# Optimization experiments

Measured on AMD Instinct MI355X. Metric: run time of the kernel, lower is better.

## Reference

```python
import jax, jax.numpy as jnp
import numpy as np

B, S, H, NH, MAXLEN = 4, 1024, 2048, 16, 1024
HD = H // NH  # head_dim = 128

def setup_inputs() -> dict:
    key = jax.random.key(0)
    ks = jax.random.split(key, 16)
    def lin(i):
        # torch Linear default init ~ U(-1/sqrt(in), 1/sqrt(in)); store W as [in, out]
        bound = 1.0 / np.sqrt(H)
        W = jax.random.uniform(ks[i], (H, H), jnp.float32, -bound, bound)
        b = jax.random.uniform(ks[i + 1], (H,), jnp.float32, -bound, bound)
        return W, b
    Wq, bq = lin(0)
    Wk, bk = lin(2)
    Wv, bv = lin(4)
    Wu, bu = lin(6)
    Wf2, bf2 = lin(8)
    rel_table = jax.random.normal(ks[10], (2 * MAXLEN - 1, NH), jnp.float32)
    query = jax.random.normal(ks[11], (B, S, H), jnp.float32)
    key_t = jax.random.normal(ks[12], (B, S, H), jnp.float32)
    value = jax.random.normal(ks[13], (B, S, H), jnp.float32)
    # causal mask [B, Sq, Sk]
    attn_mask = jnp.broadcast_to(jnp.tril(jnp.ones((S, S), bool)), (B, S, S))
    return {"query": query, "key": key_t, "value": value, "attn_mask": attn_mask,
            "Wq": Wq, "bq": bq, "Wk": Wk, "bk": bk, "Wv": Wv, "bv": bv,
            "Wu": Wu, "bu": bu, "Wf2": Wf2, "bf2": bf2, "rel_table": rel_table}

def reference(query, key, value, attn_mask, Wq, bq, Wk, bk, Wv, bv, Wu, bu, Wf2, bf2, rel_table):
    silu = jax.nn.silu
    U = silu(query @ Wu + bu)                      # [B,S,H]
    Q = silu(query @ Wq + bq).reshape(B, S, NH, HD).transpose(0, 2, 1, 3)  # [B,NH,S,HD]
    K = silu(key @ Wk + bk).reshape(B, S, NH, HD).transpose(0, 2, 1, 3)
    V = silu(value @ Wv + bv).reshape(B, S, NH, HD).transpose(0, 2, 1, 3)
    scale = HD ** -0.5
    scores = jnp.einsum('bhqd,bhkd->bhqk', Q, K) * scale  # [B,NH,S,S]
    # relative position bias lookup (non-infer path)
    positions = jnp.arange(S)[:, None] - jnp.arange(S)[None, :]
    rel_idx = positions + MAXLEN - 1                       # [S,S]
    rel_bias = rel_table[rel_idx].transpose(2, 0, 1)[None]  # [1,NH,S,S]
    scores = scores + rel_bias
    attn = silu(scores)  # SiLU attention instead of softmax
    attn = jnp.where(attn_mask[:, None, :, :], attn, 0.0)
    out = jnp.einsum('bhqk,bhkd->bhqd', attn, V)           # [B,NH,S,HD]
    out = out.transpose(0, 2, 1, 3).reshape(B, S, H)
    gated = out * U
    return gated @ Wf2 + bf2
```

## Files before the change

### kernel.cpp

```cpp
#include <hip/hip_runtime.h>
#include <stdint.h>

#define HDIM 2048
#define SEQLEN 1024
#define NHEADS 16
#define HEADD 128

typedef unsigned short u16;
typedef unsigned int u32;
typedef __attribute__((ext_vector_type(8))) short bf16x8;
typedef __attribute__((ext_vector_type(8))) u16 u16x8;
typedef __attribute__((ext_vector_type(4))) u16 u16x4;
typedef __attribute__((ext_vector_type(4))) float f32x4;

__device__ __forceinline__ float bf2f(u16 u) {
    union { u32 i; float f; } v; v.i = ((u32)u) << 16; return v.f;
}
__device__ __forceinline__ u16 f2bf(float f) {
    union { float f; u32 i; } v; v.f = f;
    return (u16)((v.i + 0x7fffu + ((v.i >> 16) & 1u)) >> 16);
}
__device__ __forceinline__ u16 f2bf_t(float f) {
    union { float f; u32 i; } v; v.f = f; return (u16)(v.i >> 16);
}
__device__ __forceinline__ float silu_f(float x) {
    return x * __builtin_amdgcn_rcpf(1.f + __expf(-x));
}
__device__ __forceinline__ void glds16(const void* g, void* l) {
    __builtin_amdgcn_global_load_lds(
        (const __attribute__((address_space(1))) u32*)g,
        (__attribute__((address_space(3))) u32*)l, 16, 0, 0);
}

__global__ __launch_bounds__(256) void f32_to_bf16(const float* __restrict__ in,
                                                   u16* __restrict__ out, int n8) {
    int i = blockIdx.x * 256 + threadIdx.x;
    const int stride = gridDim.x * 256;
    for (; i < n8; i += stride) {
        f32x4 a = *(const f32x4*)&in[(size_t)i * 8];
        f32x4 b = *(const f32x4*)&in[(size_t)i * 8 + 4];
        u16x8 o;
#pragma unroll
        for (int j = 0; j < 4; ++j) { o[j] = f2bf(a[j]); o[4 + j] = f2bf(b[j]); }
        *(u16x8*)&out[(size_t)i * 8] = o;
    }
}

__global__ __launch_bounds__(256) void transpose_w(const float* __restrict__ W,
                                                   u16* __restrict__ WT) {
    __shared__ u16 T[64][76];
    const int r0 = blockIdx.y * 64;
    const int c0 = blockIdx.x * 64;
    const int t = threadIdx.x;
#pragma unroll
    for (int c = t; c < 1024; c += 256) {
        const int r = c >> 4, cc = (c & 15) << 2;
        f32x4 v = *(const f32x4*)&W[(size_t)(r0 + r) * HDIM + c0 + cc];
        u16x4 o;
#pragma unroll
        for (int j = 0; j < 4; ++j) o[j] = f2bf(v[j]);
        *(u16x4*)&T[r][cc] = o;
    }
    __syncthreads();
#pragma unroll
    for (int c = t; c < 512; c += 256) {
        const int n = c >> 3, kc = (c & 7) << 3;
        u16x8 v;
#pragma unroll
        for (int j = 0; j < 8; ++j) v[j] = T[kc + j][n];
        *(u16x8*)&WT[(size_t)(c0 + n) * HDIM + r0 + kc] = v;
    }
}

__global__ __launch_bounds__(256) void transpose_v(const u16* __restrict__ V,
                                                   u16* __restrict__ VT) {
    __shared__ u16 T[64][76];
    const int bh = blockIdx.y;
    const int st = (blockIdx.x & 15) * 64;
    const int dt = (blockIdx.x >> 4) * 64;
    const int b = bh >> 4, h = bh & 15;
    const int t = threadIdx.x;
#pragma unroll
    for (int c = t; c < 1024; c += 256) {
        const int s = c >> 4, d4 = (c & 15) << 2;
        *(u16x4*)&T[s][d4] =
            *(const u16x4*)&V[(size_t)(b * SEQLEN + st + s) * HDIM + h * HEADD + dt + d4];
    }
    __syncthreads();
#pragma unroll
    for (int c = t; c < 512; c += 256) {
        const int d = c >> 3, s8 = (c & 7) << 3;
        u16x8 v;
#pragma unroll
        for (int j = 0; j < 8; ++j) v[j] = T[s8 + j][d];
        *(u16x8*)&VT[((size_t)bh * HEADD + dt + d) * SEQLEN + st + s8] = v;
    }
}

__global__ __launch_bounds__(512, 2) void gemm256_8p(
    const u16* __restrict__ X,
    const u16* __restrict__ WTq, const u16* __restrict__ WTu,
    const float* __restrict__ bq, const float* __restrict__ bu,
    u16* __restrict__ Qo, u16* __restrict__ Uo)
{
    extern __shared__ u16 lds[];
    const int t = threadIdx.x;
    const int lane = t & 63, wid = t >> 6;
    const int l15 = lane & 15, l4 = lane >> 4;
    const int wr = wid >> 2, wn = wid & 3;

    const int bid = blockIdx.x;
    const int u = (bid & 7) * 32 + (bid >> 3);
    const int tm = u & 15, tn = u >> 4;
    const int m0 = tm * 256;
    const int n0 = tn * 256;
    const u16* WT = (n0 < 2048) ? WTq : WTu;
    const float* bias = (n0 < 2048) ? bq : bu;
    u16* outp = (n0 < 2048) ? Qo : Uo;
    const int nc0 = n0 & 2047;

    const int r64 = t >> 3;
    const int cse = (((t & 7) ^ (r64 & 7)) << 3);
    const u16* gA = X + (size_t)(m0 + r64) * HDIM + cse;
    const int rB0 = (r64 >> 5) * 64 + (r64 & 31);
    const u16* gB = WT + (size_t)(nc0 + rB0) * HDIM + cse;

    const int wbase = wid * 512;
    const int dstBw = (wid >> 2) * 4096 + (wid & 3) * 512;

    int offA[8][2], offB[4][2];
#pragma unroll
    for (int mf = 0; mf < 8; ++mf) {
        const int row = wr * 128 + mf * 16 + l15;
#pragma unroll
        for (int kk = 0; kk < 2; ++kk) {
            const int c = kk * 4 + l4;
            offA[mf][kk] = row * 64 + (((c) ^ (row & 7)) << 3);
        }
    }
#pragma unroll
    for (int nf = 0; nf < 4; ++nf) {
        const int row = wn * 64 + nf * 16 + l15;
#pragma unroll
        for (int kk = 0; kk < 2; ++kk) {
            const int c = kk * 4 + l4;
            offB[nf][kk] = 16384 + row * 64 + (((c) ^ (row & 7)) << 3);
        }
    }

#define SA(buf, rb, kt) glds16(gA + (size_t)(rb) * HDIM + (kt) * 64, \
                               lds + (buf) * 32768 + (rb) * 64 + wbase)
#define SB(buf, c, half, kt) glds16(gB + (size_t)((c) * 128 + (half) * 32) * HDIM + (kt) * 64, \
                               lds + (buf) * 32768 + 16384 + dstBw + (c) * 8192 + (half) * 2048)

    SA(0, 0, 0);    SA(0, 128, 0);
    SB(0, 0, 0, 0); SB(0, 1, 0, 0);
    SB(0, 0, 1, 0); SB(0, 1, 1, 0);
    SA(0, 64, 0);   SA(0, 192, 0);
    asm volatile("s_waitcnt vmcnt(4)" ::: "memory");
    __builtin_amdgcn_s_barrier();

    f32x4 acc[8][4] = {};
    int cur = 0;

#pragma unroll 1
    for (int kt = 0; kt < 32; ++kt) {
        const u16* pc = lds + cur * 32768;
        const int nb = cur ^ 1;
        const bool pf = (kt + 1 < 32);
        bf16x8 a[4][2], b0[2][2], b1[2][2];

#pragma unroll
        for (int mf = 0; mf < 4; ++mf)
#pragma unroll
            for (int kk = 0; kk < 2; ++kk)
                a[mf][kk] = *(const bf16x8*)(pc + offA[mf][kk]);
#pragma unroll
        for (int nf = 0; nf < 2; ++nf)
#pragma unroll
            for (int kk = 0; kk < 2; ++kk)
                b0[nf][kk] = *(const bf16x8*)(pc + offB[nf][kk]);
        if (pf) { SA(nb, 0, kt + 1); SA(nb, 128, kt + 1); }
        __builtin_amdgcn_s_barrier();
        asm volatile("s_waitcnt lgkmcnt(0)");
        __builtin_amdgcn_sched_barrier(0);
        __builtin_amdgcn_s_setprio(1);
#pragma unroll
        for (int mf = 0; mf < 4; ++mf)
#pragma unroll
            for (int nf = 0; nf < 2; ++nf)
#pragma unroll
                for (int kk = 0; kk < 2; ++kk)
                    acc[mf][nf] = __builtin_amdgcn_mfma_f32_16x16x32_bf16(
                        a[mf][kk], b0[nf][kk], acc[mf][nf], 0, 0, 0);
        __builtin_amdgcn_s_setprio(0);
        if (pf) { asm volatile("s_waitcnt vmcnt(4)" ::: "memory"); }
        else    { asm volatile("s_waitcnt vmcnt(2)" ::: "memory"); }
        __builtin_amdgcn_s_barrier();

#pragma unroll
        for (int nf = 0; nf < 2; ++nf)
#pragma unroll
            for (int kk = 0; kk < 2; ++kk)
                b1[nf][kk] = *(const bf16x8*)(pc + offB[2 + nf][kk]);
        if (pf) { SB(nb, 0, 0, kt + 1); SB(nb, 1, 0, kt + 1); }
        __builtin_amdgcn_s_barrier();
        asm volatile("s_waitcnt lgkmcnt(0)");
        __builtin_amdgcn_sched_barrier(0);
        __builtin_amdgcn_s_setprio(1);
#pragma unroll
        for (int mf = 0; mf < 4; ++mf)
#pragma unroll
            for (int nf = 0; nf < 2; ++nf)
#pragma unroll
                for (int kk = 0; kk < 2; ++kk)
                    acc[mf][2 + nf] = __builtin_amdgcn_mfma_f32_16x16x32_bf16(
                        a[mf][kk], b1[nf][kk], acc[mf][2 + nf], 0, 0, 0);
        __builtin_amdgcn_s_setprio(0);
        if (pf) { asm volatile("s_waitcnt vmcnt(4)" ::: "memory"); }
        else    { asm volatile("s_waitcnt vmcnt(0)" ::: "memory"); }
        __builtin_amdgcn_s_barrier();

#pragma unroll
        for (int mf = 0; mf < 4; ++mf)
#pragma unroll
            for (int kk = 0; kk < 2; ++kk)
                a[mf][kk] = *(const bf16x8*)(pc + offA[4 + mf][kk]);
        if (pf) { SB(nb, 0, 1, kt + 1); SB(nb, 1, 1, kt + 1); }
        __builtin_amdgcn_s_barrier();
        asm volatile("s_waitcnt lgkmcnt(0)");
        __builtin_amdgcn_sched_barrier(0);
        __builtin_amdgcn_s_setprio(1);
#pragma unroll
        for (int mf = 0; mf < 4; ++mf)
#pragma unroll
            for (int nf = 0; nf < 2; ++nf)
#pragma unroll
                for (int kk = 0; kk < 2; ++kk)
                    acc[4 + mf][nf] = __builtin_amdgcn_mfma_f32_16x16x32_bf16(
                        a[mf][kk], b0[nf][kk], acc[4 + mf][nf], 0, 0, 0);
        __builtin_amdgcn_s_setprio(0);
        __builtin_amdgcn_s_barrier();

        if (pf) { SA(nb, 64, kt + 1); SA(nb, 192, kt + 1); }
        __builtin_amdgcn_s_barrier();
        __builtin_amdgcn_s_setprio(1);
#pragma unroll
        for (int mf = 0; mf < 4; ++mf)
#pragma unroll
            for (int nf = 0; nf < 2; ++nf)
#pragma unroll
                for (int kk = 0; kk < 2; ++kk)
                    acc[4 + mf][2 + nf] = __builtin_amdgcn_mfma_f32_16x16x32_bf16(
                        a[mf][kk], b1[nf][kk], acc[4 + mf][2 + nf], 0, 0, 0);
        __builtin_amdgcn_s_setprio(0);
        if (pf) { asm volatile("s_waitcnt vmcnt(4)" ::: "memory"); }
        __builtin_amdgcn_s_barrier();
        cur ^= 1;
    }
#undef SA
#undef SB

    float bvv[4];
#pragma unroll
    for (int nf = 0; nf < 4; ++nf) bvv[nf] = bias[nc0 + wn * 64 + nf * 16 + l15];
#pragma unroll
    for (int mf = 0; mf < 8; ++mf) {
        const int mbase = m0 + wr * 128 + mf * 16 + (l4 << 2);
#pragma unroll
        for (int r = 0; r < 4; ++r) {
            u16* rowp = outp + (size_t)(mbase + r) * HDIM + nc0 + wn * 64 + l15;
#pragma unroll
            for (int nf = 0; nf < 4; ++nf)
                rowp[nf * 16] = f2bf(silu_f(acc[mf][nf][r] + bvv[nf]));
        }
    }
}

__global__ __launch_bounds__(256) void gemm128(
    const u16* __restrict__ X, const u16* __restrict__ WT,
    const float* __restrict__ bias, void* __restrict__ outp, const int mode)
{
    extern __shared__ u16 lds[];
    const int t = threadIdx.x;
    const int lane = t & 63, wid = t >> 6;
    const int l15 = lane & 15, l4 = lane >> 4;
    const int wr = wid >> 1, wn = wid & 1;

    const int bid = blockIdx.x;
    const int u = (bid & 7) * 64 + (bid >> 3);
    const int tm = u & 31, tn = u >> 5;
    const int m0 = tm * 128, n0 = tn * 128;

    const int ric = t >> 3;
    const int cse = (((t & 7) ^ (ric & 7)) << 3);
    const u16* gA = X  + (size_t)(m0 + ric) * HDIM + cse;
    const u16* gB = WT + (size_t)(n0 + ric) * HDIM + cse;

    u16* buf0 = lds;
    u16* buf1 = lds + 16384;
    const int wbase = wid * 512;

    int offA[4][2], offB[4][2];
#pragma unroll
    for (int i = 0; i < 4; ++i) {
        const int row = wr * 64 + i * 16 + l15;
#pragma unroll
        for (int kk = 0; kk < 2; ++kk)
            offA[i][kk] = ((row * 128 + kk * 64 + l4 * 16) ^ ((row & 7) << 4)) >> 1;
    }
#pragma unroll
    for (int j = 0; j < 4; ++j) {
        const int row = wn * 64 + j * 16 + l15;
#pragma unroll
        for (int kk = 0; kk < 2; ++kk)
            offB[j][kk] = 8192 + ((((row * 128 + kk * 64 + l4 * 16) ^ ((row & 7) << 4))) >> 1);
    }

#define STAGE_A(buf, c, kt) glds16(gA + (size_t)(c) * 32 * HDIM + (kt) * 64, (buf) + (c) * 2048 + wbase)
#define STAGE_B(buf, c, kt) glds16(gB + (size_t)(c) * 32 * HDIM + (kt) * 64, (buf) + 8192 + (c) * 2048 + wbase)

    STAGE_B(buf0, 0, 0); STAGE_B(buf0, 1, 0); STAGE_B(buf0, 2, 0); STAGE_B(buf0, 3, 0);
    STAGE_A(buf0, 0, 0); STAGE_A(buf0, 1, 0); STAGE_A(buf0, 2, 0); STAGE_A(buf0, 3, 0);
    STAGE_B(buf1, 0, 1); STAGE_B(buf1, 1, 1); STAGE_B(buf1, 2, 1); STAGE_B(buf1, 3, 1);
    STAGE_A(buf1, 0, 1); STAGE_A(buf1, 2, 1);
    asm volatile("s_waitcnt vmcnt(6)" ::: "memory");
    __builtin_amdgcn_s_barrier();

    f32x4 acc[4][4] = {};
    u16* pc = buf0;
    u16* pn = buf1;

#pragma unroll 1
    for (int tt = 0; tt < 32; ++tt) {
        bf16x8 bfr[4][2], afr[2][2];
#pragma unroll
        for (int j = 0; j < 4; ++j)
#pragma unroll
            for (int kk = 0; kk < 2; ++kk)
                bfr[j][kk] = *(const bf16x8*)(pc + offB[j][kk]);
#pragma unroll
        for (int i = 0; i < 2; ++i)
#pragma unroll
            for (int kk = 0; kk < 2; ++kk)
                afr[i][kk] = *(const bf16x8*)(pc + offA[i][kk]);
        if (tt + 1 < 32) { STAGE_A(pn, 1, tt + 1); STAGE_A(pn, 3, tt + 1); }
        __builtin_amdgcn_s_barrier();
        asm volatile("s_waitcnt lgkmcnt(0)");
        __builtin_amdgcn_sched_barrier(0);
        __builtin_amdgcn_s_setprio(1);
#pragma unroll
        for (int i = 0; i < 2; ++i)
#pragma unroll
            for (int j = 0; j < 4; ++j)
#pragma unroll
                for (int kk = 0; kk < 2; ++kk)
                    acc[i][j] = __builtin_amdgcn_mfma_f32_16x16x32_bf16(
                        afr[i][kk], bfr[j][kk], acc[i][j], 0, 0, 0);
        __builtin_amdgcn_s_setprio(0);
        __builtin_amdgcn_s_barrier();

#pragma unroll
        for (int i = 0; i < 2; ++i)
#pragma unroll
            for (int kk = 0; kk < 2; ++kk)
                afr[i][kk] = *(const bf16x8*)(pc + offA[2 + i][kk]);
        if (tt + 2 < 32) {
            STAGE_B(pc, 0, tt + 2); STAGE_B(pc, 1, tt + 2);
            STAGE_B(pc, 2, tt + 2); STAGE_B(pc, 3, tt + 2);
            STAGE_A(pc, 0, tt + 2); STAGE_A(pc, 2, tt + 2);
        }
        __builtin_amdgcn_s_barrier();
        asm volatile("s_waitcnt lgkmcnt(0)");
        __builtin_amdgcn_sched_barrier(0);
        __builtin_amdgcn_s_setprio(1);
#pragma unroll
        for (int i = 0; i < 2; ++i)
#pragma unroll
            for (int j = 0; j < 4; ++j)
#pragma unroll
                for (int kk = 0; kk < 2; ++kk)
                    acc[2 + i][j] = __builtin_amdgcn_mfma_f32_16x16x32_bf16(
                        afr[i][kk], bfr[j][kk], acc[2 + i][j], 0, 0, 0);
        __builtin_amdgcn_s_setprio(0);
        if (tt + 2 < 32)      { asm volatile("s_waitcnt vmcnt(6)" ::: "memory"); }
        else if (tt + 1 < 32) { asm volatile("s_waitcnt vmcnt(0)" ::: "memory"); }
        __builtin_amdgcn_s_barrier();
        u16* tmp = pc; pc = pn; pn = tmp;
    }
#undef STAGE_A
#undef STAGE_B

    float bvv[4];
#pragma unroll
    for (int j = 0; j < 4; ++j) bvv[j] = bias[n0 + wn * 64 + j * 16 + l15];
#pragma unroll
    for (int i = 0; i < 4; ++i) {
        const int mbase = m0 + wr * 64 + i * 16 + (l4 << 2);
#pragma unroll
        for (int r = 0; r < 4; ++r) {
            const size_t rowoff = (size_t)(mbase + r) * HDIM + n0 + wn * 64 + l15;
#pragma unroll
            for (int j = 0; j < 4; ++j) {
                const float v = acc[i][j][r] + bvv[j];
                if (mode == 0)
                    ((u16*)outp)[rowoff + j * 16] = f2bf(silu_f(v));
                else
                    ((float*)outp)[rowoff + j * 16] = v;
            }
        }
    }
}

__global__ __launch_bounds__(256) void attn_fused(
    const u16* __restrict__ Qb, const u16* __restrict__ Kb,
    const u16* __restrict__ VTg, const u16* __restrict__ Ub,
    const float* __restrict__ rel, u16* __restrict__ G)
{
    extern __shared__ u16 alds[];
    u16* Ps = alds + 24576;
    float* relh = (float*)(alds + 33792);

    const int idx = blockIdx.x;
    const int bh8 = idx & 7;
    const int j = (idx >> 3) & 7;
    const int bhhi = idx >> 6;
    const int bh = bhhi * 8 + bh8;
    const int b = bh >> 4, h = bh & 15;
    const int qS0 = j * 64;
    const int qL0 = (15 - j) * 64;
    const int nkt = 16 - j;
    const int t = threadIdx.x, lane = t & 63, w = t >> 6;
    const int l15 = lane & 15, l4 = lane >> 4;
    const size_t rowbase = (size_t)b * SEQLEN;
    const int col0 = h * HEADD;
    const float scale = 0.088388347648318447f;

    for (int i = t; i < 1024; i += 256) relh[i] = rel[(size_t)(1023 + i) * NHEADS + h];

    const int rK = t >> 4;
    const int cK = (t & 15) ^ (rK & 7);
    const u16* gK = Kb + (rowbase + rK) * HDIM + col0 + cK * 8;
    const int rV = t >> 3;
    const int cV = (t & 7) ^ (rV & 7);
    const u16* gV = VTg + ((size_t)bh * HEADD + rV) * SEQLEN + cV * 8;
    const int sdst = w * 512;

    bf16x8 aqL[4], aqS[4];
    {
        const int qrowL = qL0 + w * 16 + l15;
        const int qrowS = qS0 + w * 16 + l15;
#pragma unroll
        for (int dc = 0; dc < 4; ++dc) {
            aqL[dc] = *(const bf16x8*)&Qb[(rowbase + qrowL) * HDIM + col0 + dc * 32 + (l4 << 3)];
            aqS[dc] = *(const bf16x8*)&Qb[(rowbase + qrowS) * HDIM + col0 + dc * 32 + (l4 << 3)];
        }
    }

    f32x4 oaccL[8] = {}, oaccS[8] = {};

#define STAGE_K(kt) do {                                                        \
    const size_t ko_ = (size_t)(kt) * 64;                                       \
    _Pragma("unroll") for (int c = 0; c < 4; ++c)                               \
        glds16(gK + (ko_ + c * 16) * HDIM, alds + c * 2048 + sdst);             \
} while (0)
#define STAGE_V(kt, bsel) do {                                                  \
    u16* vb_ = alds + 8192 + ((bsel) ? 8192 : 0);                               \
    const size_t ko_ = (size_t)(kt) * 64;                                       \
    _Pragma("unroll") for (int c = 0; c < 4; ++c)                               \
        glds16(gV + (size_t)c * 32 * SEQLEN + ko_, vb_ + c * 2048 + sdst);      \
} while (0)

    STAGE_K(0); STAGE_V(0, 0);
    asm volatile("s_waitcnt vmcnt(0)" ::: "memory");
    __builtin_amdgcn_s_barrier();

    int cur = 0;
#pragma unroll 1
    for (int kt = 0; kt < nkt; ++kt) {
        const int k0 = kt * 64;
        const bool doS = (kt <= j);
        if (kt + 1 < nkt) STAGE_V(kt + 1, cur ^ 1);
        const u16* kb = alds;
        const u16* vb = alds + 8192 + (cur ? 8192 : 0);

#pragma unroll
        for (int kf = 0; kf < 4; ++kf) {
            const int krow = kf * 16 + l15;
            f32x4 sL = {}, sS = {};
            __builtin_amdgcn_s_setprio(1);
#pragma unroll
            for (int dc = 0; dc < 4; ++dc) {
                bf16x8 bk = *(const bf16x8*)&kb[krow * 128 + (((dc * 4 + l4) ^ (krow & 7)) << 3)];
                sL = __builtin_amdgcn_mfma_f32_16x16x32_bf16(aqL[dc], bk, sL, 0, 0, 0);
                if (doS) sS = __builtin_amdgcn_mfma_f32_16x16x32_bf16(aqS[dc], bk, sS, 0, 0, 0);
            }
            __builtin_amdgcn_s_setprio(0);
            const int kabs = k0 + krow;
            const int prow = w * 16 + (l4 << 2);
#pragma unroll
            for (int r = 0; r < 4; ++r) {
                const int qabsL = qL0 + prow + r;
                float vL = 0.f;
                if (kabs <= qabsL) vL = silu_f(fmaf(sL[r], scale, relh[qabsL - kabs]));
                Ps[(prow + r) * 72 + kf * 16 + l15] = f2bf_t(vL);
            }
            if (doS) {
#pragma unroll
                for (int r = 0; r < 4; ++r) {
                    const int qabsS = qS0 + prow + r;
                    float vS = 0.f;
                    if (kabs <= qabsS) vS = silu_f(fmaf(sS[r], scale, relh[qabsS - kabs]));
                    Ps[(64 + prow + r) * 72 + kf * 16 + l15] = f2bf_t(vS);
                }
            }
        }
        asm volatile("s_waitcnt lgkmcnt(0)" ::: "memory");
        __builtin_amdgcn_s_barrier();
        if (kt + 1 < nkt) STAGE_K(kt + 1);

        bf16x8 apL[2], apS[2];
#pragma unroll
        for (int kc = 0; kc < 2; ++kc) {
            apL[kc] = *(const bf16x8*)&Ps[(w * 16 + l15) * 72 + kc * 32 + (l4 << 3)];
            if (doS) apS[kc] = *(const bf16x8*)&Ps[(64 + w * 16 + l15) * 72 + kc * 32 + (l4 << 3)];
        }
        __builtin_amdgcn_s_setprio(1);
#pragma unroll
        for (int df = 0; df < 8; ++df) {
            const int vrow = df * 16 + l15;
#pragma unroll
            for (int kc = 0; kc < 2; ++kc) {
                bf16x8 bv = *(const bf16x8*)&vb[vrow * 64 + (((kc * 4 + l4) ^ (vrow & 7)) << 3)];
                oaccL[df] = __builtin_amdgcn_mfma_f32_16x16x32_bf16(apL[kc], bv, oaccL[df], 0, 0, 0);
                if (doS) oaccS[df] = __builtin_amdgcn_mfma_f32_16x16x32_bf16(apS[kc], bv, oaccS[df], 0, 0, 0);
            }
        }
        __builtin_amdgcn_s_setprio(0);
        asm volatile("s_waitcnt vmcnt(0) lgkmcnt(0)" ::: "memory");
        __builtin_amdgcn_s_barrier();
        cur ^= 1;
    }
#undef STAGE_K
#undef STAGE_V

#pragma unroll
    for (int r = 0; r < 4; ++r) {
        const int qr = w * 16 + (l4 << 2) + r;
        const size_t rowL = (rowbase + qL0 + qr) * HDIM + col0 + l15;
        const size_t rowS = (rowbase + qS0 + qr) * HDIM + col0 + l15;
#pragma unroll
        for (int df = 0; df < 8; ++df)
            G[rowL + df * 16] = f2bf(oaccL[df][r] * bf2f(Ub[rowL + df * 16]));
#pragma unroll
        for (int df = 0; df < 8; ++df)
            G[rowS + df * 16] = f2bf(oaccS[df][r] * bf2f(Ub[rowS + df * 16]));
    }
}

extern "C" void kernel_launch(void* const* d_in, const int* in_sizes, int n_in,
                              void* d_out, int out_size, void* d_ws, size_t ws_size,
                              hipStream_t stream) {
    const float* query = (const float*)d_in[0];
    const float* key_  = (const float*)d_in[1];
    const float* value = (const float*)d_in[2];
    const float* Wq  = (const float*)d_in[4];  const float* bq  = (const float*)d_in[5];
    const float* Wk  = (const float*)d_in[6];  const float* bk  = (const float*)d_in[7];
    const float* Wv  = (const float*)d_in[8];  const float* bv  = (const float*)d_in[9];
    const float* Wu  = (const float*)d_in[10]; const float* bu  = (const float*)d_in[11];
    const float* Wf2 = (const float*)d_in[12]; const float* bf2 = (const float*)d_in[13];
    const float* rel = (const float*)d_in[14];

    char* ws = (char*)d_ws;
    const size_t WBYTES = (size_t)HDIM * HDIM * 2;
    const size_t ABYTES = (size_t)4096 * HDIM * 2;
    u16* WTa  = (u16*)ws;
    u16* Xbf  = (u16*)(ws + WBYTES);
    u16* Qbuf = (u16*)(ws + WBYTES + 1 * ABYTES);
    u16* Kbuf = (u16*)(ws + WBYTES + 2 * ABYTES);
    u16* Vbuf = (u16*)(ws + WBYTES + 3 * ABYTES);
    u16* Ubuf = (u16*)(ws + WBYTES + 4 * ABYTES);
    u16* WTb  = Vbuf;
    u16* Gbuf = Qbuf;
    u16* VTg  = Xbf;

    dim3 tpb(256);
    dim3 tgrid(32, 32);
    dim3 vgrid(32, 64);
    const int n8 = 4096 * HDIM / 8;
    const size_t GLDS  = 65536;
    const size_t G8LDS = 131072;
    const size_t ALDS  = 71680;

    f32_to_bf16<<<2048, tpb, 0, stream>>>(query, Xbf, n8);
    transpose_w<<<tgrid, tpb, 0, stream>>>(Wq, WTa);
    transpose_w<<<tgrid, tpb, 0, stream>>>(Wu, WTb);
    gemm256_8p<<<256, 512, G8LDS, stream>>>(Xbf, WTa, WTb, bq, bu, Qbuf, Ubuf);
    transpose_w<<<tgrid, tpb, 0, stream>>>(Wk, WTa);
    f32_to_bf16<<<2048, tpb, 0, stream>>>(key_, Xbf, n8);
    gemm128<<<512, tpb, GLDS, stream>>>(Xbf, WTa, bk, Kbuf, 0);
    transpose_w<<<tgrid, tpb, 0, stream>>>(Wv, WTa);
    f32_to_bf16<<<2048, tpb, 0, stream>>>(value, Xbf, n8);
    gemm128<<<512, tpb, GLDS, stream>>>(Xbf, WTa, bv, Vbuf, 0);
    transpose_v<<<vgrid, tpb, 0, stream>>>(Vbuf, VTg);
    attn_fused<<<512, tpb, ALDS, stream>>>(Qbuf, Kbuf, VTg, Ubuf, rel, Gbuf);
    transpose_w<<<tgrid, tpb, 0, stream>>>(Wf2, WTa);
    gemm128<<<512, tpb, GLDS, stream>>>(Gbuf, WTa, bf2, d_out, 1);
}
```

Measured before the change: 330.6 us.

## Split attention L/S query tiles across separate waves with 512-thread blocks

The attention kernel now uses 8 waves per block instead of 4. Waves 0-3 handle the long (late) query tile and waves 4-7 handle the short (early) tile, where before each wave interleaved both. This halves per-wave accumulator and Q register state and gives more latency hiding per CU. The staging of K and V is redistributed across 512 threads. The cost is that S-tile waves go idle at barriers once their causal range ends, and two block-wide barriers per iteration now synchronise twice as many waves.

Result: faster. 320.0 us (-3.2%).

```diff
diff --git a/kernel.cpp b/kernel.cpp
--- a/kernel.cpp
+++ b/kernel.cpp
@@ -412,7 +412,7 @@
     }
 }
 
-__global__ __launch_bounds__(256) void attn_fused(
+__global__ __launch_bounds__(512) void attn_fused(
     const u16* __restrict__ Qb, const u16* __restrict__ Kb,
     const u16* __restrict__ VTg, const u16* __restrict__ Ub,
     const float* __restrict__ rel, u16* __restrict__ G)
@@ -431,44 +431,39 @@
     const int qL0 = (15 - j) * 64;
     const int nkt = 16 - j;
     const int t = threadIdx.x, lane = t & 63, w = t >> 6;
-    const int l15 = lane & 15, l4 = lane >> 4;
+    const int wq = w & 3;
+    const bool isL = (w < 4);
+    const int l15 = lane & 15, l4 = lane >> 4, l3 = lane >> 3;
     const size_t rowbase = (size_t)b * SEQLEN;
     const int col0 = h * HEADD;
     const float scale = 0.088388347648318447f;
 
-    for (int i = t; i < 1024; i += 256) relh[i] = rel[(size_t)(1023 + i) * NHEADS + h];
-
-    const int rK = t >> 4;
-    const int cK = (t & 15) ^ (rK & 7);
-    const u16* gK = Kb + (rowbase + rK) * HDIM + col0 + cK * 8;
-    const int rV = t >> 3;
-    const int cV = (t & 7) ^ (rV & 7);
-    const u16* gV = VTg + ((size_t)bh * HEADD + rV) * SEQLEN + cV * 8;
-    const int sdst = w * 512;
-
-    bf16x8 aqL[4], aqS[4];
-    {
-        const int qrowL = qL0 + w * 16 + l15;
-        const int qrowS = qS0 + w * 16 + l15;
-#pragma unroll
-        for (int dc = 0; dc < 4; ++dc) {
-            aqL[dc] = *(const bf16x8*)&Qb[(rowbase + qrowL) * HDIM + col0 + dc * 32 + (l4 << 3)];
-            aqS[dc] = *(const bf16x8*)&Qb[(rowbase + qrowS) * HDIM + col0 + dc * 32 + (l4 << 3)];
-        }
-    }
-
-    f32x4 oaccL[8] = {}, oaccS[8] = {};
+    for (int i = t; i < 1024; i += 512) relh[i] = rel[(size_t)(1023 + i) * NHEADS + h];
+
+    const u16* gK0 = Kb + (rowbase + w * 8 + l4) * HDIM + col0 + ((lane & 15) ^ l4) * 8;
+    const u16* gK1 = Kb + (rowbase + w * 8 + 4 + l4) * HDIM + col0 + ((lane & 15) ^ (l4 + 4)) * 8;
+    const u16* gV0 = VTg + ((size_t)bh * HEADD + w * 16 + l3) * SEQLEN + ((lane & 7) ^ l3) * 8;
+    const u16* gV1 = VTg + ((size_t)bh * HEADD + w * 16 + 8 + l3) * SEQLEN + ((lane & 7) ^ l3) * 8;
+
+    const int q0 = (isL ? qL0 : qS0) + wq * 16;
+    bf16x8 aq[4];
+#pragma unroll
+    for (int dc = 0; dc < 4; ++dc)
+        aq[dc] = *(const bf16x8*)&Qb[(rowbase + q0 + l15) * HDIM + col0 + dc * 32 + (l4 << 3)];
+
+    f32x4 oacc[8] = {};
+    const int prB = (isL ? 0 : 64) + wq * 16;
 
 #define STAGE_K(kt) do {                                                        \
-    const size_t ko_ = (size_t)(kt) * 64;                                       \
-    _Pragma("unroll") for (int c = 0; c < 4; ++c)                               \
-        glds16(gK + (ko_ + c * 16) * HDIM, alds + c * 2048 + sdst);             \
+    const size_t ko_ = (size_t)(kt) * 64 * HDIM;                                \
+    glds16(gK0 + ko_, alds + w * 1024);                                         \
+    glds16(gK1 + ko_, alds + w * 1024 + 512);                                   \
 } while (0)
 #define STAGE_V(kt, bsel) do {                                                  \
     u16* vb_ = alds + 8192 + ((bsel) ? 8192 : 0);                               \
     const size_t ko_ = (size_t)(kt) * 64;                                       \
-    _Pragma("unroll") for (int c = 0; c < 4; ++c)                               \
-        glds16(gV + (size_t)c * 32 * SEQLEN + ko_, vb_ + c * 2048 + sdst);      \
+    glds16(gV0 + ko_, vb_ + w * 1024);                                          \
+    glds16(gV1 + ko_, vb_ + w * 1024 + 512);                                    \
 } while (0)
 
     STAGE_K(0); STAGE_V(0, 0);
@@ -479,64 +474,55 @@
 #pragma unroll 1
     for (int kt = 0; kt < nkt; ++kt) {
         const int k0 = kt * 64;
-        const bool doS = (kt <= j);
+        const bool act = isL || (kt <= j);
         if (kt + 1 < nkt) STAGE_V(kt + 1, cur ^ 1);
         const u16* kb = alds;
         const u16* vb = alds + 8192 + (cur ? 8192 : 0);
 
-#pragma unroll
-        for (int kf = 0; kf < 4; ++kf) {
-            const int krow = kf * 16 + l15;
-            f32x4 sL = {}, sS = {};
+        if (act) {
+#pragma unroll
+            for (int kf = 0; kf < 4; ++kf) {
+                const int krow = kf * 16 + l15;
+                f32x4 s = {};
+                __builtin_amdgcn_s_setprio(1);
+#pragma unroll
+                for (int dc = 0; dc < 4; ++dc) {
+                    bf16x8 bk = *(const bf16x8*)&kb[krow * 128 + (((dc * 4 + l4) ^ (krow & 7)) << 3)];
+                    s = __builtin_amdgcn_mfma_f32_16x16x32_bf16(aq[dc], bk, s, 0, 0, 0);
+                }
+                __builtin_amdgcn_s_setprio(0);
+                const int kabs = k0 + krow;
+                const int pr = prB + (l4 << 2);
+#pragma unroll
+                for (int r = 0; r < 4; ++r) {
+                    const int qabs = q0 + (l4 << 2) + r;
+                    float v = 0.f;
+                    if (kabs <= qabs) v = silu_f(fmaf(s[r], scale, relh[qabs - kabs]));
+                    Ps[(pr + r) * 72 + kf * 16 + l15] = f2bf_t(v);
+                }
+            }
+        }
+        asm volatile("s_waitcnt lgkmcnt(0)" ::: "memory");
+        __builtin_amdgcn_s_barrier();
+        if (kt + 1 < nkt) STAGE_K(kt + 1);
+
+        if (act) {
+            bf16x8 ap[2];
+#pragma unroll
+            for (int kc = 0; kc < 2; ++kc)
+                ap[kc] = *(const bf16x8*)&Ps[(prB + l15) * 72 + kc * 32 + (l4 << 3)];
             __builtin_amdgcn_s_setprio(1);
 #pragma unroll
-            for (int dc = 0; dc < 4; ++dc) {
-                bf16x8 bk = *(const bf16x8*)&kb[krow * 128 + (((dc * 4 + l4) ^ (krow & 7)) << 3)];
-                sL = __builtin_amdgcn_mfma_f32_16x16x32_bf16(aqL[dc], bk, sL, 0, 0, 0);
-                if (doS) sS = __builtin_amdgcn_mfma_f32_16x16x32_bf16(aqS[dc], bk, sS, 0, 0, 0);
+            for (int df = 0; df < 8; ++df) {
+                const int vrow = df * 16 + l15;
+#pragma unroll
+                for (int kc = 0; kc < 2; ++kc) {
+                    bf16x8 bv = *(const bf16x8*)&vb[vrow * 64 + (((kc * 4 + l4) ^ (vrow & 7)) << 3)];
+                    oacc[df] = __builtin_amdgcn_mfma_f32_16x16x32_bf16(ap[kc], bv, oacc[df], 0, 0, 0);
+                }
             }
             __builtin_amdgcn_s_setprio(0);
-            const int kabs = k0 + krow;
-            const int prow = w * 16 + (l4 << 2);
-#pragma unroll
-            for (int r = 0; r < 4; ++r) {
-                const int qabsL = qL0 + prow + r;
-                float vL = 0.f;
-                if (kabs <= qabsL) vL = silu_f(fmaf(sL[r], scale, relh[qabsL - kabs]));
-                Ps[(prow + r) * 72 + kf * 16 + l15] = f2bf_t(vL);
-            }
-            if (doS) {
-#pragma unroll
-                for (int r = 0; r < 4; ++r) {
-                    const int qabsS = qS0 + prow + r;
-                    float vS = 0.f;
-                    if (kabs <= qabsS) vS = silu_f(fmaf(sS[r], scale, relh[qabsS - kabs]));
-                    Ps[(64 + prow + r) * 72 + kf * 16 + l15] = f2bf_t(vS);
-                }
-            }
-        }
-        asm volatile("s_waitcnt lgkmcnt(0)" ::: "memory");
-        __builtin_amdgcn_s_barrier();
-        if (kt + 1 < nkt) STAGE_K(kt + 1);
-
-        bf16x8 apL[2], apS[2];
-#pragma unroll
-        for (int kc = 0; kc < 2; ++kc) {
-            apL[kc] = *(const bf16x8*)&Ps[(w * 16 + l15) * 72 + kc * 32 + (l4 << 3)];
-            if (doS) apS[kc] = *(const bf16x8*)&Ps[(64 + w * 16 + l15) * 72 + kc * 32 + (l4 << 3)];
-        }
-        __builtin_amdgcn_s_setprio(1);
-#pragma unroll
-        for (int df = 0; df < 8; ++df) {
-            const int vrow = df * 16 + l15;
-#pragma unroll
-            for (int kc = 0; kc < 2; ++kc) {
-                bf16x8 bv = *(const bf16x8*)&vb[vrow * 64 + (((kc * 4 + l4) ^ (vrow & 7)) << 3)];
-                oaccL[df] = __builtin_amdgcn_mfma_f32_16x16x32_bf16(apL[kc], bv, oaccL[df], 0, 0, 0);
-                if (doS) oaccS[df] = __builtin_amdgcn_mfma_f32_16x16x32_bf16(apS[kc], bv, oaccS[df], 0, 0, 0);
-            }
-        }
-        __builtin_amdgcn_s_setprio(0);
+        }
         asm volatile("s_waitcnt vmcnt(0) lgkmcnt(0)" ::: "memory");
         __builtin_amdgcn_s_barrier();
         cur ^= 1;
@@ -546,15 +532,11 @@
 
 #pragma unroll
     for (int r = 0; r < 4; ++r) {
-        const int qr = w * 16 + (l4 << 2) + r;
-        const size_t rowL = (rowbase + qL0 + qr) * HDIM + col0 + l15;
-        const size_t rowS = (rowbase + qS0 + qr) * HDIM + col0 + l15;
+        const int qr = q0 + (l4 << 2) + r;
+        const size_t row = (rowbase + qr) * HDIM + col0 + l15;
 #pragma unroll
         for (int df = 0; df < 8; ++df)
-            G[rowL + df * 16] = f2bf(oaccL[df][r] * bf2f(Ub[rowL + df * 16]));
-#pragma unroll
-        for (int df = 0; df < 8; ++df)
-            G[rowS + df * 16] = f2bf(oaccS[df][r] * bf2f(Ub[rowS + df * 16]));
+            G[row + df * 16] = f2bf(oacc[df][r] * bf2f(Ub[row + df * 16]));
     }
 }
 
@@ -603,7 +585,7 @@
     f32_to_bf16<<<2048, tpb, 0, stream>>>(value, Xbf, n8);
     gemm128<<<512, tpb, GLDS, stream>>>(Xbf, WTa, bv, Vbuf, 0);
     transpose_v<<<vgrid, tpb, 0, stream>>>(Vbuf, VTg);
-    attn_fused<<<512, tpb, ALDS, stream>>>(Qbuf, Kbuf, VTg, Ubuf, rel, Gbuf);
+    attn_fused<<<512, 512, ALDS, stream>>>(Qbuf, Kbuf, VTg, Ubuf, rel, Gbuf);
     transpose_w<<<tgrid, tpb, 0, stream>>>(Wf2, WTa);
     gemm128<<<512, tpb, GLDS, stream>>>(Gbuf, WTa, bf2, d_out, 1);
 }
```
